# Performance work log

Measured on AMD Instinct MI355X. Metric: run time of the kernel, lower is better.

Reference implementation:

```python
import jax, jax.numpy as jnp
import numpy as np

DMODEL = 1024
N_EXPERTS = 8
EXPERT_SIZE = 4096
TOPK = 2
B, S = 2, 2048


def setup_inputs() -> dict:
    key = jax.random.key(0)
    ks = jax.random.split(key, 6)
    std = EXPERT_SIZE ** (-0.5)  # init_expert_weights: normal(0, expert_size**-0.5 * weight_scale)
    x = jax.random.normal(ks[0], (B, S, DMODEL), dtype=jnp.float32)
    gate_w = 0.02 * jax.random.normal(ks[1], (N_EXPERTS, DMODEL), dtype=jnp.float32)
    w1 = std * jax.random.normal(ks[2], (N_EXPERTS, EXPERT_SIZE, DMODEL), dtype=jnp.float32)
    b1 = jnp.zeros((N_EXPERTS, EXPERT_SIZE), dtype=jnp.float32)
    w2 = std * jax.random.normal(ks[3], (N_EXPERTS, DMODEL, EXPERT_SIZE), dtype=jnp.float32)
    b2 = jnp.zeros((N_EXPERTS, DMODEL), dtype=jnp.float32)
    return {"x": x, "gate_w": gate_w, "w1": w1, "b1": b1, "w2": w2, "b2": b2}


def reference(x, gate_w, w1, b1, w2, b2):
    # Router: gate linear (no bias) -> softmax -> top-k expert selection
    logits = jnp.einsum('bsd,ed->bse', x, gate_w)          # [B,S,E]
    probs = jax.nn.softmax(logits, axis=-1)                # gate_softmax
    top_w, top_i = jax.lax.top_k(probs, TOPK)              # [B,S,K]
    # Scatter top-k weights back to a dense [B,S,E] routing matrix
    route = jnp.sum(jax.nn.one_hot(top_i, N_EXPERTS, dtype=probs.dtype)
                    * top_w[..., None], axis=-2)           # [B,S,E]
    # Per-expert 2-layer MLP (Linear -> ReLU -> Linear), combined by route weights
    out = jnp.zeros_like(x)
    for e in range(N_EXPERTS):
        h = jax.nn.relu(jnp.einsum('bsd,hd->bsh', x, w1[e]) + b1[e])  # [B,S,H]
        y = jnp.einsum('bsh,dh->bsd', h, w2[e]) + b2[e]               # [B,S,D]
        out = out + route[..., e, None] * y
    return out
```

## Files before the change

### kernel.cpp

```cpp
#include <hip/hip_runtime.h>
#include <hip/hip_bf16.h>
#include <stdint.h>

#define DMODEL 1024
#define NEXP   8
#define HSZ    4096
#define NTOK   4096
#define KSPLIT 2

typedef __attribute__((ext_vector_type(8))) short bf16x8;
typedef __attribute__((ext_vector_type(4))) float f32x4;

__device__ __forceinline__ unsigned short f2bf(float f) {
  union { float f; unsigned u; } v; v.f = f;
  return (unsigned short)((v.u + 0x8000u) >> 16);
}

__device__ __forceinline__ void gl2lds16(const void* g, void* lds) {
  __builtin_amdgcn_global_load_lds(
      (const __attribute__((address_space(1))) unsigned*)g,
      (__attribute__((address_space(3))) unsigned*)lds, 16, 0, 0);
}

__global__ __launch_bounds__(256) void cvt_all_kernel(
    const float* __restrict__ w1, const float* __restrict__ w2,
    unsigned short* __restrict__ w1b, unsigned short* __restrict__ w2b) {
  const size_t n1 = (size_t)NEXP * HSZ * DMODEL / 4;
  size_t i = (size_t)blockIdx.x * 256 + threadIdx.x;
  const float* src; unsigned short* dst; size_t j;
  if (i < n1) { src = w1; dst = w1b; j = i; }
  else        { src = w2; dst = w2b; j = i - n1; }
  float4 v = ((const float4*)src)[j];
  ((ushort4*)dst)[j] = make_ushort4(f2bf(v.x), f2bf(v.y), f2bf(v.z), f2bf(v.w));
}

__global__ __launch_bounds__(256) void router_kernel(
    const float* __restrict__ x, const float* __restrict__ gw,
    int* __restrict__ cnt, int* __restrict__ tokl, float* __restrict__ twgt,
    int* __restrict__ sidx, unsigned short* __restrict__ xb) {
  __shared__ int lcnt[NEXP];
  __shared__ int lbase[NEXP];
  __shared__ int rE[32];
  __shared__ int rS[32];
  __shared__ float rW[32];
  const int tid = threadIdx.x;
  const int wave = tid >> 6;
  const int lane = tid & 63;
  if (tid < NEXP) lcnt[tid] = 0;
  __syncthreads();

  for (int i = 0; i < 4; ++i) {
    int lt = wave * 4 + i;
    int t = blockIdx.x * 16 + lt;
    const float* xr = x + (size_t)t * DMODEL;
    unsigned short* xbr = xb + (size_t)t * DMODEL;
    float acc[NEXP];
#pragma unroll
    for (int e = 0; e < NEXP; ++e) acc[e] = 0.f;
    for (int d = lane; d < DMODEL; d += 64) {
      float xv = xr[d];
      xbr[d] = f2bf(xv);
#pragma unroll
      for (int e = 0; e < NEXP; ++e) acc[e] = fmaf(xv, gw[e * DMODEL + d], acc[e]);
    }
#pragma unroll
    for (int e = 0; e < NEXP; ++e) {
#pragma unroll
      for (int o = 32; o > 0; o >>= 1) acc[e] += __shfl_down(acc[e], o);
    }
    if (lane == 0) {
      float m = acc[0];
#pragma unroll
      for (int e = 1; e < NEXP; ++e) m = fmaxf(m, acc[e]);
      float p[NEXP]; float s = 0.f;
#pragma unroll
      for (int e = 0; e < NEXP; ++e) { p[e] = __expf(acc[e] - m); s += p[e]; }
      float inv = 1.f / s;
      int i0 = 0; float b0 = p[0];
#pragma unroll
      for (int e = 1; e < NEXP; ++e) if (p[e] > b0) { b0 = p[e]; i0 = e; }
      int i1 = (i0 == 0) ? 1 : 0; float b1v = p[i1];
#pragma unroll
      for (int e = 0; e < NEXP; ++e) if (e != i0 && p[e] > b1v) { b1v = p[e]; i1 = e; }
      int s0l = atomicAdd(&lcnt[i0], 1);
      rE[lt * 2] = i0; rS[lt * 2] = s0l; rW[lt * 2] = b0 * inv;
      int s1l = atomicAdd(&lcnt[i1], 1);
      rE[lt * 2 + 1] = i1; rS[lt * 2 + 1] = s1l; rW[lt * 2 + 1] = b1v * inv;
    }
  }
  __syncthreads();
  if (tid < NEXP) lbase[tid] = atomicAdd(&cnt[tid], lcnt[tid]);
  __syncthreads();
  if (tid < 32) {
    int e = rE[tid];
    int p = lbase[e] + rS[tid];
    int t = blockIdx.x * 16 + (tid >> 1);
    tokl[e * NTOK + p] = t;
    twgt[e * NTOK + p] = rW[tid];
    sidx[2 * t + (tid & 1)] = (e << 16) | p;
  }
}


#define SOFF(buf, mat, half) (((buf) * 4 + (mat) * 2 + (half)) * 8192)

#define STG_A(buf, half, kt) do { if ((kt) < NSTEP) {                         \
    gl2lds16(aP[half][0] + (size_t)(kt) * 64, &SH[SOFF(buf,0,half) + (w*16)*64]);     \
    gl2lds16(aP[half][1] + (size_t)(kt) * 64, &SH[SOFF(buf,0,half) + (w*16+8)*64]); } } while(0)

#define STG_B(buf, half, kt) do { if ((kt) < NSTEP) {                         \
    gl2lds16(bP + (size_t)((half)*128) * Bstr + (size_t)(kt) * 64, &SH[SOFF(buf,1,half) + (w*16)*64]);   \
    gl2lds16(bP + (size_t)((half)*128+8) * Bstr + (size_t)(kt) * 64, &SH[SOFF(buf,1,half) + (w*16+8)*64]); } } while(0)

#define RD_A(dst, buf, half) do {                                             \
    dst[0][0] = *(const bf16x8*)&SH[SOFF(buf,0,half) + aoff[0][0]];           \
    dst[0][1] = *(const bf16x8*)&SH[SOFF(buf,0,half) + aoff[0][1]];           \
    dst[1][0] = *(const bf16x8*)&SH[SOFF(buf,0,half) + aoff[1][0]];           \
    dst[1][1] = *(const bf16x8*)&SH[SOFF(buf,0,half) + aoff[1][1]]; } while(0)

#define RD_B(dst, buf, half) do {                                             \
    _Pragma("unroll") for (int j_ = 0; j_ < 4; ++j_) {                        \
      dst[j_][0] = *(const bf16x8*)&SH[SOFF(buf,1,half) + boff[j_][0]];       \
      dst[j_][1] = *(const bf16x8*)&SH[SOFF(buf,1,half) + boff[j_][1]]; } } while(0)

#define MFMA_Q(q, a, b) do {                                                  \
    _Pragma("unroll") for (int i_ = 0; i_ < 2; ++i_)                          \
    _Pragma("unroll") for (int j_ = 0; j_ < 4; ++j_)                          \
    _Pragma("unroll") for (int k_ = 0; k_ < 2; ++k_)                          \
      acc[q][i_][j_] = __builtin_amdgcn_mfma_f32_16x16x32_bf16(               \
          b[j_][k_], a[i_][k_], acc[q][i_][j_], 0, 0, 0); } while(0)

#define PH_COMPUTE(q, a, b)                                                   \
    __builtin_amdgcn_s_barrier();                                             \
    asm volatile("s_waitcnt lgkmcnt(0)" ::: "memory");                        \
    __builtin_amdgcn_sched_barrier(0);                                        \
    __builtin_amdgcn_s_setprio(1);                                            \
    MFMA_Q(q, a, b);                                                          \
    __builtin_amdgcn_s_setprio(0);                                            \
    __builtin_amdgcn_sched_barrier(0);                                        \
    __builtin_amdgcn_s_barrier();

#define KTILE(buf, t) do {                                                    \
                                                             \
    RD_A(a0f, buf, 0); RD_B(b0f, buf, 0);                                     \
    STG_B(buf ^ 1, 1, (t) + 1);                                               \
    PH_COMPUTE(0, a0f, b0f)                                                   \
                                                             \
    RD_B(b1f, buf, 1);                                                        \
    STG_A(buf, 0, (t) + 2);                                                   \
    PH_COMPUTE(1, a0f, b1f)                                                   \
                                                             \
    RD_A(a1f, buf, 1);                                                        \
    STG_B(buf, 0, (t) + 2);                                                   \
    PH_COMPUTE(2, a1f, b0f)                                                   \
                                            \
    STG_A(buf, 1, (t) + 2);                                                   \
    __builtin_amdgcn_s_barrier();                                             \
    asm volatile("s_waitcnt lgkmcnt(0)" ::: "memory");                        \
    __builtin_amdgcn_sched_barrier(0);                                        \
    __builtin_amdgcn_s_setprio(1);                                            \
    MFMA_Q(3, a1f, b1f);                                                      \
    __builtin_amdgcn_s_setprio(0);                                            \
    __builtin_amdgcn_sched_barrier(0);                                        \
    if ((t) < NSTEP - 2) asm volatile("s_waitcnt vmcnt(6)" ::: "memory");     \
    else                 asm volatile("s_waitcnt vmcnt(0)" ::: "memory");     \
    __builtin_amdgcn_s_barrier();                                             \
  } while(0)

#define GEMM_PROLOGUE()                                                       \
    STG_A(0, 0, 0); STG_B(0, 0, 0); STG_A(0, 1, 0); STG_B(0, 1, 0);           \
    STG_A(1, 0, 1); STG_B(1, 0, 1); STG_A(1, 1, 1);                           \
    asm volatile("s_waitcnt vmcnt(6)" ::: "memory");                          \
    __builtin_amdgcn_s_barrier();

__global__ __launch_bounds__(512) void gemm1_bf_kernel(
    const unsigned short* __restrict__ Xbf, const unsigned short* __restrict__ W1bf,
    const float* __restrict__ b1, const int* __restrict__ cnt,
    const int* __restrict__ tokl, unsigned short* __restrict__ Hbuf) {
  const int b = blockIdx.x + 16 * blockIdx.y + 256 * blockIdx.z;
  const int xcd = b & 7;
  const int slot = b >> 3;
  const int c = xcd + 8 * (slot >> 4);
  const int wx = c & 15, wz = c >> 4, wy = slot & 15;

  const int e = wz;
  const int ne = cnt[e];
  const int m0 = wy * 256;
  if (m0 >= ne) return;
  const int n0 = wx * 256;
  int toff = 0;
  for (int i = 0; i < NEXP; ++i) toff += (i < e) ? cnt[i] : 0;

  __shared__ __align__(16) unsigned short SH[65536];

  const int tid = threadIdx.x;
  const int lane = tid & 63;
  const int w = tid >> 6;
  const int aw = w >> 1;
  const int bw = w & 1;
  const int fr = lane & 15;
  const int cb0 = lane >> 4;

  constexpr int NSTEP = DMODEL / 64;
  const size_t Bstr = DMODEL;

  const int srow8 = lane >> 3;
  const int sswz = ((lane & 7) ^ srow8) * 8;
  const int* tlist = tokl + e * NTOK;
  const unsigned short* aP[2][2];
#pragma unroll
  for (int h = 0; h < 2; ++h)
#pragma unroll
    for (int cc = 0; cc < 2; ++cc) {
      int gr = m0 + h * 128 + w * 16 + cc * 8 + srow8;
      int tk = tlist[(gr < ne) ? gr : 0];
      aP[h][cc] = Xbf + (size_t)tk * DMODEL + sswz;
    }
  const unsigned short* bP = W1bf + (size_t)e * HSZ * DMODEL
      + (size_t)(n0 + w * 16 + srow8) * DMODEL + sswz;

  int aoff[2][2], boff[4][2];
#pragma unroll
  for (int i = 0; i < 2; ++i)
#pragma unroll
    for (int kk = 0; kk < 2; ++kk) {
      int rr = aw * 32 + i * 16 + fr;
      aoff[i][kk] = rr * 64 + (((kk * 4 + cb0) ^ (fr & 7)) * 8);
    }
#pragma unroll
  for (int j = 0; j < 4; ++j)
#pragma unroll
    for (int kk = 0; kk < 2; ++kk) {
      int rr = bw * 64 + j * 16 + fr;
      boff[j][kk] = rr * 64 + (((kk * 4 + cb0) ^ (fr & 7)) * 8);
    }

  f32x4 acc[4][2][4];
#pragma unroll
  for (int q = 0; q < 4; ++q)
#pragma unroll
    for (int i = 0; i < 2; ++i)
#pragma unroll
      for (int j = 0; j < 4; ++j) acc[q][i][j] = (f32x4){0.f, 0.f, 0.f, 0.f};

  bf16x8 a0f[2][2], a1f[2][2], b0f[4][2], b1f[4][2];

  GEMM_PROLOGUE()
  for (int t = 0; t < NSTEP; t += 2) {
    KTILE(0, t);
    KTILE(1, t + 1);
  }

  const int dq = cb0 * 4;
#pragma unroll
  for (int q = 0; q < 4; ++q) {
    const int qm = q >> 1, qn = q & 1;
#pragma unroll
    for (int i = 0; i < 2; ++i) {
      int trow = m0 + qm * 128 + aw * 32 + i * 16 + fr;
      if (trow >= ne) continue;
      size_t hrow = (size_t)(toff + trow) * HSZ;
#pragma unroll
      for (int j = 0; j < 4; ++j) {
        int hcol = n0 + qn * 128 + bw * 64 + j * 16 + dq;
        const float* bp = b1 + e * HSZ + hcol;
        unsigned short u[4];
#pragma unroll
        for (int r = 0; r < 4; ++r)
          u[r] = f2bf(fmaxf(acc[q][i][j][r] + bp[r], 0.f));
        *(ushort4*)&Hbuf[hrow + hcol] = make_ushort4(u[0], u[1], u[2], u[3]);
      }
    }
  }
}

__global__ __launch_bounds__(512) void gemm2_bf_kernel(
    const unsigned short* __restrict__ Hbuf, const unsigned short* __restrict__ W2bf,
    const int* __restrict__ cnt, const float* __restrict__ twgt,
    float* __restrict__ Ybuf) {
  const int b = blockIdx.x + 4 * blockIdx.y + 64 * blockIdx.z;
  const int xcd = b & 7;
  const int slot = b >> 3;
  const int c = xcd + 8 * (slot >> 4);
  const int wx = c & 3, wz = c >> 2, wy = slot & 15;

  const int e = wz & 7;
  const int ks = wz >> 3;
  const int ne = cnt[e];
  const int m0 = wy * 256;
  if (m0 >= ne) return;
  const int n0 = wx * 256;
  const int kbase = ks * (HSZ / KSPLIT);
  int toff = 0;
  for (int i = 0; i < NEXP; ++i) toff += (i < e) ? cnt[i] : 0;

  __shared__ __align__(16) unsigned short SH[65536];

  const int tid = threadIdx.x;
  const int lane = tid & 63;
  const int w = tid >> 6;
  const int aw = w >> 1;
  const int bw = w & 1;
  const int fr = lane & 15;
  const int cb0 = lane >> 4;

  constexpr int NSTEP = (HSZ / KSPLIT) / 64;
  const size_t Bstr = HSZ;

  const int srow8 = lane >> 3;
  const int sswz = ((lane & 7) ^ srow8) * 8;
  const unsigned short* aP[2][2];
#pragma unroll
  for (int h = 0; h < 2; ++h)
#pragma unroll
    for (int cc = 0; cc < 2; ++cc) {
      int gr = m0 + h * 128 + w * 16 + cc * 8 + srow8;
      int rc = (gr < ne) ? gr : 0;
      aP[h][cc] = Hbuf + (size_t)(toff + rc) * HSZ + kbase + sswz;
    }
  const unsigned short* bP = W2bf + (size_t)e * DMODEL * HSZ
      + (size_t)(n0 + w * 16 + srow8) * HSZ + kbase + sswz;

  int aoff[2][2], boff[4][2];
#pragma unroll
  for (int i = 0; i < 2; ++i)
#pragma unroll
    for (int kk = 0; kk < 2; ++kk) {
      int rr = aw * 32 + i * 16 + fr;
      aoff[i][kk] = rr * 64 + (((kk * 4 + cb0) ^ (fr & 7)) * 8);
    }
#pragma unroll
  for (int j = 0; j < 4; ++j)
#pragma unroll
    for (int kk = 0; kk < 2; ++kk) {
      int rr = bw * 64 + j * 16 + fr;
      boff[j][kk] = rr * 64 + (((kk * 4 + cb0) ^ (fr & 7)) * 8);
    }

  f32x4 acc[4][2][4];
#pragma unroll
  for (int q = 0; q < 4; ++q)
#pragma unroll
    for (int i = 0; i < 2; ++i)
#pragma unroll
      for (int j = 0; j < 4; ++j) acc[q][i][j] = (f32x4){0.f, 0.f, 0.f, 0.f};

  bf16x8 a0f[2][2], a1f[2][2], b0f[4][2], b1f[4][2];

  GEMM_PROLOGUE()
  for (int t = 0; t < NSTEP; t += 2) {
    KTILE(0, t);
    KTILE(1, t + 1);
  }

  const float* wlist = twgt + e * NTOK;
  float* yp = Ybuf + (size_t)ks * (2 * NTOK) * DMODEL;
  const int dq = cb0 * 4;
#pragma unroll
  for (int q = 0; q < 4; ++q) {
    const int qm = q >> 1, qn = q & 1;
#pragma unroll
    for (int i = 0; i < 2; ++i) {
      int trow = m0 + qm * 128 + aw * 32 + i * 16 + fr;
      if (trow >= ne) continue;
      float wgt = wlist[trow];
      float* yrow = yp + (size_t)(toff + trow) * DMODEL;
#pragma unroll
      for (int j = 0; j < 4; ++j) {
        int d0 = n0 + qn * 128 + bw * 64 + j * 16 + dq;
        float4 v = make_float4(wgt * acc[q][i][j][0], wgt * acc[q][i][j][1],
                               wgt * acc[q][i][j][2], wgt * acc[q][i][j][3]);
        *(float4*)(yrow + d0) = v;
      }
    }
  }
}

__global__ __launch_bounds__(256) void combine_kernel(
    const float* __restrict__ Ybuf, const float* __restrict__ b2,
    const int* __restrict__ cnt, const int* __restrict__ sidx,
    const float* __restrict__ twgt, float* __restrict__ out) {
  int t = blockIdx.x;
  int offv[NEXP];
  int s = 0;
#pragma unroll
  for (int e = 0; e < NEXP; ++e) { offv[e] = s; s += cnt[e]; }
  int s0 = sidx[2 * t], s1 = sidx[2 * t + 1];
  int e0 = s0 >> 16, e1 = s1 >> 16;
  int sl0 = s0 & 0xffff, sl1 = s1 & 0xffff;
  size_t r0 = (size_t)(offv[e0] + sl0) * DMODEL;
  size_t r1 = (size_t)(offv[e1] + sl1) * DMODEL;
  float w0 = twgt[e0 * NTOK + sl0];
  float w1 = twgt[e1 * NTOK + sl1];
  const size_t PSTR = (size_t)(2 * NTOK) * DMODEL;
  int c = threadIdx.x * 4;
  float4 a0 = *(const float4*)(Ybuf + r0 + c);
  float4 a1 = *(const float4*)(Ybuf + PSTR + r0 + c);
  float4 c0 = *(const float4*)(Ybuf + r1 + c);
  float4 c1 = *(const float4*)(Ybuf + PSTR + r1 + c);
  float4 bb0 = *(const float4*)(b2 + (size_t)e0 * DMODEL + c);
  float4 bb1 = *(const float4*)(b2 + (size_t)e1 * DMODEL + c);
  *(float4*)(out + (size_t)t * DMODEL + c) = make_float4(
      a0.x + a1.x + c0.x + c1.x + w0 * bb0.x + w1 * bb1.x,
      a0.y + a1.y + c0.y + c1.y + w0 * bb0.y + w1 * bb1.y,
      a0.z + a1.z + c0.z + c1.z + w0 * bb0.z + w1 * bb1.z,
      a0.w + a1.w + c0.w + c1.w + w0 * bb0.w + w1 * bb1.w);
}

extern "C" void kernel_launch(void* const* d_in, const int* in_sizes, int n_in,
                              void* d_out, int out_size, void* d_ws, size_t ws_size,
                              hipStream_t stream) {
  const float* x  = (const float*)d_in[0];
  const float* gw = (const float*)d_in[1];
  const float* w1 = (const float*)d_in[2];
  const float* b1 = (const float*)d_in[3];
  const float* w2 = (const float*)d_in[4];
  const float* b2 = (const float*)d_in[5];
  float* out = (float*)d_out;

  char* ws = (char*)d_ws;
  int* cnt    = (int*)ws;
  int* tokl   = (int*)(ws + 128);
  float* twgt = (float*)(ws + 128 + NEXP * NTOK * 4);
  int* sidx   = (int*)(ws + 128 + 2 * NEXP * NTOK * 4);

  constexpr size_t OFF_XBF  = 327680;
  constexpr size_t OFF_W1BF = OFF_XBF  + (size_t)NTOK * DMODEL * 2;
  constexpr size_t OFF_W2BF = OFF_W1BF + (size_t)NEXP * HSZ * DMODEL * 2;
  constexpr size_t OFF_HBUF = OFF_W2BF + (size_t)NEXP * DMODEL * HSZ * 2;
  unsigned short* Xbf  = (unsigned short*)(ws + OFF_XBF);
  unsigned short* W1bf = (unsigned short*)(ws + OFF_W1BF);
  unsigned short* W2bf = (unsigned short*)(ws + OFF_W2BF);
  unsigned short* Hbuf = (unsigned short*)(ws + OFF_HBUF);
  float* Ybuf = (float*)(ws + OFF_W1BF);

  hipMemsetAsync(cnt, 0, 32, stream);
  router_kernel<<<NTOK / 16, 256, 0, stream>>>(x, gw, cnt, tokl, twgt, sidx, Xbf);
  const size_t ncvt = 2 * (size_t)NEXP * HSZ * DMODEL / 4;
  cvt_all_kernel<<<(unsigned)((ncvt + 255) / 256), 256, 0, stream>>>(
      w1, w2, W1bf, W2bf);
  gemm1_bf_kernel<<<dim3(HSZ / 256, NTOK / 256, NEXP), 512, 0, stream>>>(
      Xbf, W1bf, b1, cnt, tokl, Hbuf);
  gemm2_bf_kernel<<<dim3(DMODEL / 256, NTOK / 256, NEXP * KSPLIT), 512, 0, stream>>>(
      Hbuf, W2bf, cnt, twgt, Ybuf);
  combine_kernel<<<NTOK, 256, 0, stream>>>(Ybuf, b2, cnt, sidx, twgt, out);
}
```

Measured before the change: 579.9 us.

## Relax GEMM k-tile barriers and vectorize router loads

The GEMM k-tile loop drops the explicit lgkmcnt waits and sched_barriers and cuts the per-phase double barriers to one barrier per phase. It also hoists the second B-fragment LDS read to the start of the tile so the compiler can overlap LDS reads with MFMAs. The router now loads x and gate weights as float4 and writes bf16 as ushort4, which cuts the number of memory instructions. The reduced synchronization could allow overlapping LDS reads and async stores to race if the compiler's implicit waits are insufficient, and holding more fragments live raises register pressure.

Result: faster. 551.5 us (-4.9%).

```diff
diff --git a/kernel.cpp b/kernel.cpp
--- a/kernel.cpp
+++ b/kernel.cpp
@@ -52,16 +52,24 @@
   for (int i = 0; i < 4; ++i) {
     int lt = wave * 4 + i;
     int t = blockIdx.x * 16 + lt;
-    const float* xr = x + (size_t)t * DMODEL;
-    unsigned short* xbr = xb + (size_t)t * DMODEL;
+    const float4* xr = (const float4*)(x + (size_t)t * DMODEL);
+    ushort4* xbr = (ushort4*)(xb + (size_t)t * DMODEL);
     float acc[NEXP];
 #pragma unroll
     for (int e = 0; e < NEXP; ++e) acc[e] = 0.f;
-    for (int d = lane; d < DMODEL; d += 64) {
-      float xv = xr[d];
-      xbr[d] = f2bf(xv);
-#pragma unroll
-      for (int e = 0; e < NEXP; ++e) acc[e] = fmaf(xv, gw[e * DMODEL + d], acc[e]);
+#pragma unroll
+    for (int d4 = 0; d4 < DMODEL / 4 / 64; ++d4) {
+      int idx = d4 * 64 + lane;
+      float4 xv = xr[idx];
+      xbr[idx] = make_ushort4(f2bf(xv.x), f2bf(xv.y), f2bf(xv.z), f2bf(xv.w));
+#pragma unroll
+      for (int e = 0; e < NEXP; ++e) {
+        float4 gv = ((const float4*)(gw + e * DMODEL))[idx];
+        acc[e] = fmaf(xv.x, gv.x, acc[e]);
+        acc[e] = fmaf(xv.y, gv.y, acc[e]);
+        acc[e] = fmaf(xv.z, gv.z, acc[e]);
+        acc[e] = fmaf(xv.w, gv.w, acc[e]);
+      }
     }
 #pragma unroll
     for (int e = 0; e < NEXP; ++e) {
@@ -130,41 +138,31 @@
       acc[q][i_][j_] = __builtin_amdgcn_mfma_f32_16x16x32_bf16(               \
           b[j_][k_], a[i_][k_], acc[q][i_][j_], 0, 0, 0); } while(0)
 
-#define PH_COMPUTE(q, a, b)                                                   \
-    __builtin_amdgcn_s_barrier();                                             \
-    asm volatile("s_waitcnt lgkmcnt(0)" ::: "memory");                        \
-    __builtin_amdgcn_sched_barrier(0);                                        \
+#define MFMA_PRIO(q, a, b)                                                    \
     __builtin_amdgcn_s_setprio(1);                                            \
     MFMA_Q(q, a, b);                                                          \
-    __builtin_amdgcn_s_setprio(0);                                            \
-    __builtin_amdgcn_sched_barrier(0);                                        \
-    __builtin_amdgcn_s_barrier();
+    __builtin_amdgcn_s_setprio(0);
+
+#define BAR() do { asm volatile("" ::: "memory");                             \
+    __builtin_amdgcn_s_barrier(); asm volatile("" ::: "memory"); } while(0)
 
 #define KTILE(buf, t) do {                                                    \
-                                                             \
-    RD_A(a0f, buf, 0); RD_B(b0f, buf, 0);                                     \
+    RD_A(a0f, buf, 0); RD_B(b0f, buf, 0); RD_B(b1f, buf, 1);                  \
     STG_B(buf ^ 1, 1, (t) + 1);                                               \
-    PH_COMPUTE(0, a0f, b0f)                                                   \
-                                                             \
-    RD_B(b1f, buf, 1);                                                        \
+    MFMA_PRIO(0, a0f, b0f)                                                    \
+    BAR();                                                                    \
+    RD_A(a1f, buf, 1);                                                        \
     STG_A(buf, 0, (t) + 2);                                                   \
-    PH_COMPUTE(1, a0f, b1f)                                                   \
-                                                             \
-    RD_A(a1f, buf, 1);                                                        \
+    MFMA_PRIO(1, a0f, b1f)                                                    \
+    BAR();                                                                    \
     STG_B(buf, 0, (t) + 2);                                                   \
-    PH_COMPUTE(2, a1f, b0f)                                                   \
-                                            \
+    MFMA_PRIO(2, a1f, b0f)                                                    \
+    BAR();                                                                    \
     STG_A(buf, 1, (t) + 2);                                                   \
-    __builtin_amdgcn_s_barrier();                                             \
-    asm volatile("s_waitcnt lgkmcnt(0)" ::: "memory");                        \
-    __builtin_amdgcn_sched_barrier(0);                                        \
-    __builtin_amdgcn_s_setprio(1);                                            \
-    MFMA_Q(3, a1f, b1f);                                                      \
-    __builtin_amdgcn_s_setprio(0);                                            \
-    __builtin_amdgcn_sched_barrier(0);                                        \
+    MFMA_PRIO(3, a1f, b1f)                                                    \
     if ((t) < NSTEP - 2) asm volatile("s_waitcnt vmcnt(6)" ::: "memory");     \
     else                 asm volatile("s_waitcnt vmcnt(0)" ::: "memory");     \
-    __builtin_amdgcn_s_barrier();                                             \
+    BAR();                                                                    \
   } while(0)
 
 #define GEMM_PROLOGUE()                                                       \
```
